# Kernel tuning notes

Measured on AMD Instinct MI355X. Metric: run time of the kernel, lower is better.

The kernel has to match this reference:

```python
import jax, jax.numpy as jnp
import numpy as np

# dims
B, N, D, H, L = 2, 4096, 768, 12, 2
DH = D // H          # 64, equals BigBird block_size
BS = 64              # block size
NB = N // BS         # 64 blocks
R = 3                # num_random_blocks
FF = 4 * D
EPS = 1e-12          # BigBird layer_norm_eps


def _ln(x, g, b):
    mu = jnp.mean(x, -1, keepdims=True)
    var = jnp.mean(jnp.square(x - mu), -1, keepdims=True)
    return (x - mu) * jax.lax.rsqrt(var + EPS) * g + b


def _gelu_new(x):
    c = np.sqrt(2.0 / np.pi).astype(np.float32)
    return 0.5 * x * (1.0 + jnp.tanh(c * (x + 0.044715 * x * x * x)))


def _block_sparse_attn(q, k, v, rb):
    # q,k,v: [B,H,N,DH]; rb: [H,NB,R] random block ids (constant)
    scale = 1.0 / np.sqrt(DH).astype(np.float32)
    qb = q.reshape(B, H, NB, BS, DH)
    kb = k.reshape(B, H, NB, BS, DH)
    vb = v.reshape(B, H, NB, BS, DH)
    M = NB - 2
    mids = jnp.arange(1, NB - 1)
    win = jnp.stack([mids - 1, mids, mids + 1], -1)                    # [M,3]
    glb = jnp.broadcast_to(jnp.array([0, NB - 1], jnp.int32), (M, 2))  # [M,2]
    idx = jnp.concatenate([
        jnp.broadcast_to(glb[None], (H, M, 2)),
        jnp.broadcast_to(win[None], (H, M, 3)),
        rb[:, 1:NB - 1, :]], axis=-1)                                  # [H,M,8]
    hh = jnp.arange(H)[:, None, None]
    # gather key/value blocks: [B,H,M,8,BS,DH] -> [B,H,M,512,DH]
    kg = kb[:, hh, idx].reshape(B, H, M, -1, DH)
    vg = vb[:, hh, idx].reshape(B, H, M, -1, DH)
    qm = qb[:, :, 1:NB - 1]                                            # [B,H,M,BS,DH]
    s = jnp.einsum('bhmqd,bhmkd->bhmqk', qm, kg) * scale
    cm = jnp.einsum('bhmqk,bhmkd->bhmqd', jax.nn.softmax(s, -1), vg)
    # first and last query blocks attend globally (full attention)
    qe = jnp.stack([qb[:, :, 0], qb[:, :, -1]], 2)                     # [B,H,2,BS,DH]
    se = jnp.einsum('bheqd,bhkd->bheqk', qe, k) * scale
    ce = jnp.einsum('bheqk,bhkd->bheqd', jax.nn.softmax(se, -1), v)
    out = jnp.concatenate([ce[:, :, :1], cm, ce[:, :, 1:]], axis=2)    # [B,H,NB,BS,DH]
    return out.reshape(B, H, N, DH)


def _forward(inputs_embeds, rand_blocks, pos_emb, tt_emb, emb_ln_g, emb_ln_b,
             Wq, bq, Wk, bk, Wv, bv, Wo, bo, ln1_g, ln1_b,
             Wi, bi, Wd, bd, ln2_g, ln2_b, fc_w, fc_b):
    x = inputs_embeds + pos_emb[None] + tt_emb                         # embeddings (token_type id 0)
    x = _ln(x, emb_ln_g, emb_ln_b)
    for l in range(L):
        q = (x @ Wq[l] + bq[l]).reshape(B, N, H, DH).transpose(0, 2, 1, 3)
        k = (x @ Wk[l] + bk[l]).reshape(B, N, H, DH).transpose(0, 2, 1, 3)
        v = (x @ Wv[l] + bv[l]).reshape(B, N, H, DH).transpose(0, 2, 1, 3)
        ctx = _block_sparse_attn(q, k, v, rand_blocks[l])
        ctx = ctx.transpose(0, 2, 1, 3).reshape(B, N, D)
        a = _ln(x + ctx @ Wo[l] + bo[l], ln1_g[l], ln1_b[l])
        h = _gelu_new(a @ Wi[l] + bi[l])
        x = _ln(a + h @ Wd[l] + bd[l], ln2_g[l], ln2_b[l])
    pooled = jnp.mean(x, axis=1)                                       # [B,D]; dropout is identity at eval
    return (pooled @ fc_w + fc_b).squeeze()                            # [B]


def setup_inputs() -> dict:
    key = jax.random.key(0)
    ks = jax.random.split(key, 24)
    s = 0.02
    nrm = lambda k, shp: jax.random.normal(k, shp, jnp.float32) * s
    return {
        'inputs_embeds': jax.random.normal(ks[0], (B, N, D), jnp.float32),
        'rand_blocks': jax.random.randint(ks[1], (L, H, NB, R), 0, NB, jnp.int32),
        'pos_emb': nrm(ks[2], (N, D)),
        'tt_emb': nrm(ks[3], (D,)),
        'emb_ln_g': jnp.ones((D,), jnp.float32), 'emb_ln_b': jnp.zeros((D,), jnp.float32),
        'Wq': nrm(ks[4], (L, D, D)), 'bq': jnp.zeros((L, D), jnp.float32),
        'Wk': nrm(ks[5], (L, D, D)), 'bk': jnp.zeros((L, D), jnp.float32),
        'Wv': nrm(ks[6], (L, D, D)), 'bv': jnp.zeros((L, D), jnp.float32),
        'Wo': nrm(ks[7], (L, D, D)), 'bo': jnp.zeros((L, D), jnp.float32),
        'ln1_g': jnp.ones((L, D), jnp.float32), 'ln1_b': jnp.zeros((L, D), jnp.float32),
        'Wi': nrm(ks[8], (L, D, FF)), 'bi': jnp.zeros((L, FF), jnp.float32),
        'Wd': nrm(ks[9], (L, FF, D)), 'bd': jnp.zeros((L, D), jnp.float32),
        'ln2_g': jnp.ones((L, D), jnp.float32), 'ln2_b': jnp.zeros((L, D), jnp.float32),
        'fc_w': nrm(ks[10], (D, 1)), 'fc_b': jnp.zeros((1,), jnp.float32),
    }


def reference(inputs_embeds, rand_blocks, pos_emb, tt_emb, emb_ln_g, emb_ln_b,
              Wq, bq, Wk, bk, Wv, bv, Wo, bo, ln1_g, ln1_b,
              Wi, bi, Wd, bd, ln2_g, ln2_b, fc_w, fc_b):
    return _forward(inputs_embeds, rand_blocks, pos_emb, tt_emb, emb_ln_g, emb_ln_b,
                    Wq, bq, Wk, bk, Wv, bv, Wo, bo, ln1_g, ln1_b,
                    Wi, bi, Wd, bd, ln2_g, ln2_b, fc_w, fc_b)
```

## Files before the change

kernel.cpp:

```cpp
#include <hip/hip_runtime.h>
#include <math.h>

#define B_ 2
#define N_ 4096
#define D_ 768
#define H_ 12
#define DH_ 64
#define NB_ 64
#define FF_ 3072
#define LAYERS_ 2
#define ROWS_ (B_ * N_)

typedef __attribute__((ext_vector_type(8))) short s16x8;
typedef __attribute__((ext_vector_type(8))) unsigned short u16x8;
typedef __attribute__((ext_vector_type(4))) float f32x4;

typedef const __attribute__((address_space(1))) unsigned int ga_u32;
typedef __attribute__((address_space(3))) unsigned int lds_u32;

static __device__ __forceinline__ float gelu_fast(float x) {
    float z2 = 1.5957691216057308f * x * (1.0f + 0.044715f * x * x);
    return x * __builtin_amdgcn_rcpf(1.0f + __expf(-z2));
}

static __device__ __forceinline__ unsigned bf16_rne(float f) {
    unsigned u = __float_as_uint(f);
    return (u + 0x7FFFu + ((u >> 16) & 1u)) >> 16;
}
static __device__ __forceinline__ float bfh2f(unsigned short h) {
    return __uint_as_float(((unsigned)h) << 16);
}

__global__ __launch_bounds__(256)
void prep_weights(const float* __restrict__ Wq, const float* __restrict__ Wk,
                  const float* __restrict__ Wv, const float* __restrict__ Wo,
                  const float* __restrict__ Wi, const float* __restrict__ Wd,
                  unsigned short* __restrict__ Wt) {
    const size_t LW = 7077888;
    int bid = blockIdx.x;
    int l = bid / 1728, r = bid % 1728;
    const float* W; unsigned short* T; int K, N, t, nx;
    if (r < 576) {
        int which = r / 144; t = r % 144; nx = 12; K = 768; N = 768;
        W = (which == 0 ? Wq : which == 1 ? Wk : which == 2 ? Wv : Wo) + (size_t)l * D_ * D_;
        T = Wt + l * LW + (size_t)(which < 3 ? which * 768 * 768 : 2304 * 768);
    } else if (r < 1152) {
        t = r - 576; nx = 48; K = 768; N = 3072;
        W = Wi + (size_t)l * D_ * FF_;
        T = Wt + l * LW + (size_t)(2304 * 768 + 768 * 768);
    } else {
        t = r - 1152; nx = 12; K = 3072; N = 768;
        W = Wd + (size_t)l * FF_ * D_;
        T = Wt + l * LW + (size_t)(2304 * 768 + 768 * 768 + 3072 * 768);
    }
    const int bx = t % nx, by = t / nx;
    __shared__ unsigned short tile[64][72];
    const int k0 = by * 64, n0 = bx * 64;
    const int tt = threadIdx.x;
    const int rr = tt >> 2, c0 = (tt & 3) * 16;
    const float* src = W + (size_t)(k0 + rr) * N + n0 + c0;
#pragma unroll
    for (int j = 0; j < 4; ++j) {
        float4 v = *(const float4*)(src + j * 4);
        tile[rr][c0 + j * 4 + 0] = (unsigned short)bf16_rne(v.x);
        tile[rr][c0 + j * 4 + 1] = (unsigned short)bf16_rne(v.y);
        tile[rr][c0 + j * 4 + 2] = (unsigned short)bf16_rne(v.z);
        tile[rr][c0 + j * 4 + 3] = (unsigned short)bf16_rne(v.w);
    }
    __syncthreads();
    const int nr = tt >> 2, kc = (tt & 3) * 16;
    unsigned short* dst = T + (size_t)(n0 + nr) * K + k0 + kc;
    ushort4 o;
#pragma unroll
    for (int j = 0; j < 4; ++j) {
        o.x = tile[kc + j * 4 + 0][nr];
        o.y = tile[kc + j * 4 + 1][nr];
        o.z = tile[kc + j * 4 + 2][nr];
        o.w = tile[kc + j * 4 + 3][nr];
        *(ushort4*)(dst + j * 4) = o;
    }
}

template <int OMODE>
__global__ __launch_bounds__(256)
void gemm_bt(const unsigned short* __restrict__ A, const unsigned short* __restrict__ Bt,
             const float* __restrict__ bias, void* __restrict__ Cv,
             int N, int K, int gelu) {
    __shared__ __align__(16) unsigned short smem[2 * 8192];
    const int tid = threadIdx.x, lane = tid & 63, wid = tid >> 6;
    const int bid = blockIdx.x;
    const int row0 = (bid & 63) * 128, col0 = (bid >> 6) * 128;
    const int rh = (wid >> 1) * 64, ch = (wid & 1) * 64;
    const int fr = lane & 15, fq = lane >> 4;
    const int srow = wid * 32 + (lane >> 2);
    const int skoff = (lane & 3) * 8;
    const unsigned short* gA0 = A + (size_t)(row0 + srow) * K + skoff;
    const unsigned short* gA1 = gA0 + (size_t)16 * K;
    const unsigned short* gB0 = Bt + (size_t)(col0 + srow) * K + skoff;
    const unsigned short* gB1 = gB0 + (size_t)16 * K;

    f32x4 acc[4][4] = {};
    const int nk = K >> 5;
    {
        unsigned short* s = smem;
        __builtin_amdgcn_global_load_lds((ga_u32*)gA0, (lds_u32*)&s[wid * 1024], 16, 0, 0);
        __builtin_amdgcn_global_load_lds((ga_u32*)gA1, (lds_u32*)&s[wid * 1024 + 512], 16, 0, 0);
        __builtin_amdgcn_global_load_lds((ga_u32*)gB0, (lds_u32*)&s[4096 + wid * 1024], 16, 0, 0);
        __builtin_amdgcn_global_load_lds((ga_u32*)gB1, (lds_u32*)&s[4096 + wid * 1024 + 512], 16, 0, 0);
    }
    for (int kt = 0; kt < nk; ++kt) {
        __syncthreads();
        if (kt + 1 < nk) {
            int k0 = (kt + 1) << 5;
            unsigned short* s = smem + ((kt + 1) & 1) * 8192;
            __builtin_amdgcn_global_load_lds((ga_u32*)(gA0 + k0), (lds_u32*)&s[wid * 1024], 16, 0, 0);
            __builtin_amdgcn_global_load_lds((ga_u32*)(gA1 + k0), (lds_u32*)&s[wid * 1024 + 512], 16, 0, 0);
            __builtin_amdgcn_global_load_lds((ga_u32*)(gB0 + k0), (lds_u32*)&s[4096 + wid * 1024], 16, 0, 0);
            __builtin_amdgcn_global_load_lds((ga_u32*)(gB1 + k0), (lds_u32*)&s[4096 + wid * 1024 + 512], 16, 0, 0);
        }
        const unsigned short* sA = smem + (kt & 1) * 8192;
        const unsigned short* sB = sA + 4096;
        s16x8 af[4], bf[4];
#pragma unroll
        for (int i = 0; i < 4; ++i)
            af[i] = *(const s16x8*)&sA[(rh + 16 * i + fr) * 32 + fq * 8];
#pragma unroll
        for (int j = 0; j < 4; ++j)
            bf[j] = *(const s16x8*)&sB[(ch + 16 * j + fr) * 32 + fq * 8];
#pragma unroll
        for (int i = 0; i < 4; ++i)
#pragma unroll
            for (int j = 0; j < 4; ++j)
                acc[i][j] = __builtin_amdgcn_mfma_f32_16x16x32_bf16(af[i], bf[j], acc[i][j], 0, 0, 0);
    }
    if (OMODE == 0) {
#pragma unroll
        for (int j = 0; j < 4; ++j) {
            int col = col0 + ch + 16 * j + fr;
            float bb = bias[col];
#pragma unroll
            for (int i = 0; i < 4; ++i)
#pragma unroll
                for (int r = 0; r < 4; ++r) {
                    int row = row0 + rh + 16 * i + fq * 4 + r;
                    float v = acc[i][j][r] + bb;
                    if (gelu) v = gelu_fast(v);
                    ((float*)Cv)[(size_t)row * N + col] = v;
                }
        }
    } else {
        unsigned short* sC = smem;
#pragma unroll
        for (int hh = 0; hh < 2; ++hh) {
            __syncthreads();
            if ((wid >> 1) == hh) {
#pragma unroll
                for (int j = 0; j < 4; ++j) {
                    float bb = bias[col0 + ch + 16 * j + fr];
#pragma unroll
                    for (int i = 0; i < 4; ++i)
#pragma unroll
                        for (int r = 0; r < 4; ++r) {
                            float v = acc[i][j][r] + bb;
                            if (gelu) v = gelu_fast(v);
                            sC[(16 * i + fq * 4 + r) * 136 + ch + 16 * j + fr] =
                                (unsigned short)bf16_rne(v);
                        }
                }
            }
            __syncthreads();
#pragma unroll
            for (int p = 0; p < 4; ++p) {
                int seg = p * 256 + tid;
                int r = seg >> 4, c8 = (seg & 15) * 8;
                *(u16x8*)&((unsigned short*)Cv)[(size_t)(row0 + hh * 64 + r) * N + col0 + c8] =
                    *(const u16x8*)&sC[r * 136 + c8];
            }
        }
    }
}

__global__ __launch_bounds__(256)
void gemm_qkv(const unsigned short* __restrict__ A, const unsigned short* __restrict__ Bt,
              const float* __restrict__ bq, const float* __restrict__ bk,
              const float* __restrict__ bv,
              unsigned short* __restrict__ Qh, unsigned short* __restrict__ Kh,
              unsigned short* __restrict__ VT) {
    const int K = D_;
    __shared__ __align__(16) unsigned short smem[2 * 8192];
    const int tid = threadIdx.x, lane = tid & 63, wid = tid >> 6;
    const int bid = blockIdx.x;
    const int row0 = (bid & 63) * 128;
    const int bx = bid >> 6;
    const int col0 = bx * 128;
    const int rh = (wid >> 1) * 64, ch = (wid & 1) * 64;
    const int fr = lane & 15, fq = lane >> 4;
    const int srow = wid * 32 + (lane >> 2);
    const int skoff = (lane & 3) * 8;
    const unsigned short* gA0 = A + (size_t)(row0 + srow) * K + skoff;
    const unsigned short* gA1 = gA0 + (size_t)16 * K;
    const unsigned short* gB0 = Bt + (size_t)(col0 + srow) * K + skoff;
    const unsigned short* gB1 = gB0 + (size_t)16 * K;

    f32x4 acc[4][4] = {};
    const int nk = K >> 5;
    {
        unsigned short* s = smem;
        __builtin_amdgcn_global_load_lds((ga_u32*)gA0, (lds_u32*)&s[wid * 1024], 16, 0, 0);
        __builtin_amdgcn_global_load_lds((ga_u32*)gA1, (lds_u32*)&s[wid * 1024 + 512], 16, 0, 0);
        __builtin_amdgcn_global_load_lds((ga_u32*)gB0, (lds_u32*)&s[4096 + wid * 1024], 16, 0, 0);
        __builtin_amdgcn_global_load_lds((ga_u32*)gB1, (lds_u32*)&s[4096 + wid * 1024 + 512], 16, 0, 0);
    }
    for (int kt = 0; kt < nk; ++kt) {
        __syncthreads();
        if (kt + 1 < nk) {
            int k0 = (kt + 1) << 5;
            unsigned short* s = smem + ((kt + 1) & 1) * 8192;
            __builtin_amdgcn_global_load_lds((ga_u32*)(gA0 + k0), (lds_u32*)&s[wid * 1024], 16, 0, 0);
            __builtin_amdgcn_global_load_lds((ga_u32*)(gA1 + k0), (lds_u32*)&s[wid * 1024 + 512], 16, 0, 0);
            __builtin_amdgcn_global_load_lds((ga_u32*)(gB0 + k0), (lds_u32*)&s[4096 + wid * 1024], 16, 0, 0);
            __builtin_amdgcn_global_load_lds((ga_u32*)(gB1 + k0), (lds_u32*)&s[4096 + wid * 1024 + 512], 16, 0, 0);
        }
        const unsigned short* sA = smem + (kt & 1) * 8192;
        const unsigned short* sB = sA + 4096;
        s16x8 af[4], bf[4];
#pragma unroll
        for (int i = 0; i < 4; ++i)
            af[i] = *(const s16x8*)&sA[(rh + 16 * i + fr) * 32 + fq * 8];
#pragma unroll
        for (int j = 0; j < 4; ++j)
            bf[j] = *(const s16x8*)&sB[(ch + 16 * j + fr) * 32 + fq * 8];
#pragma unroll
        for (int i = 0; i < 4; ++i)
#pragma unroll
            for (int j = 0; j < 4; ++j)
                acc[i][j] = __builtin_amdgcn_mfma_f32_16x16x32_bf16(af[i], bf[j], acc[i][j], 0, 0, 0);
    }
    const int seg = bx / 6;
    const int colbase = col0 - seg * D_;
    const float* bias = (seg == 0) ? bq : (seg == 1) ? bk : bv;
    if (seg == 2) {
#pragma unroll
        for (int j = 0; j < 4; ++j) {
            int col_l = colbase + ch + 16 * j + fr;
            float bb = bias[col_l];
#pragma unroll
            for (int i = 0; i < 4; ++i) {
                int rowbase = row0 + rh + 16 * i + fq * 4;
                ushort4 o;
                o.x = (unsigned short)bf16_rne(acc[i][j][0] + bb);
                o.y = (unsigned short)bf16_rne(acc[i][j][1] + bb);
                o.z = (unsigned short)bf16_rne(acc[i][j][2] + bb);
                o.w = (unsigned short)bf16_rne(acc[i][j][3] + bb);
                *(ushort4*)&VT[(size_t)col_l * ROWS_ + rowbase] = o;
            }
        }
    } else {
        unsigned short* dst = (seg == 0) ? Qh : Kh;
        unsigned short* sC = smem;
#pragma unroll
        for (int hh = 0; hh < 2; ++hh) {
            __syncthreads();
            if ((wid >> 1) == hh) {
#pragma unroll
                for (int j = 0; j < 4; ++j) {
                    float bb = bias[colbase + ch + 16 * j + fr];
#pragma unroll
                    for (int i = 0; i < 4; ++i)
#pragma unroll
                        for (int r = 0; r < 4; ++r)
                            sC[(16 * i + fq * 4 + r) * 136 + ch + 16 * j + fr] =
                                (unsigned short)bf16_rne(acc[i][j][r] + bb);
                }
            }
            __syncthreads();
#pragma unroll
            for (int p = 0; p < 4; ++p) {
                int seg2 = p * 256 + tid;
                int r = seg2 >> 4, c8 = (seg2 & 15) * 8;
                *(u16x8*)&dst[(size_t)(row0 + hh * 64 + r) * D_ + colbase + c8] =
                    *(const u16x8*)&sC[r * 136 + c8];
            }
        }
    }
}

template <bool EDGE>
__global__ __launch_bounds__(256, 4)
void attn_mfma(const unsigned short* __restrict__ Qb, const unsigned short* __restrict__ Kb,
               const unsigned short* __restrict__ VTb, const int* __restrict__ rb,
               unsigned short* __restrict__ ctx, float* __restrict__ scratch) {
    __shared__ __align__(16) unsigned short sQ[64][72];
    __shared__ __align__(16) unsigned short sK[64][72];
    __shared__ __align__(16) unsigned short sVT[64][72];
    __shared__ __align__(16) unsigned short sP[4][16][72];
    __shared__ int sList[16];
    const int tid = threadIdx.x, lane = tid & 63, wid = tid >> 6;
    const int fr = lane & 15, fq = lane >> 4;
    int qb, h, b, nkb, slice = 0;
    if (EDGE) {
        int part = blockIdx.x & 3;
        int hh = (blockIdx.x >> 2) % H_;
        int be = (blockIdx.x >> 2) / H_;
        int eb = be & 1;
        b = be >> 1;
        h = hh;
        qb = eb ? (NB_ - 1) : 0;
        nkb = 16;
        slice = ((b * 2 + eb) * H_ + h) * 4 + part;
        if (tid < 16) sList[tid] = part * 16 + tid;
    } else {
        qb = blockIdx.x % (NB_ - 2) + 1;
        h = (blockIdx.x / (NB_ - 2)) % H_;
        b = blockIdx.x / ((NB_ - 2) * H_);
        nkb = 8;
        if (tid < 8) {
            int e;
            if (tid == 0) e = 0;
            else if (tid == 1) e = NB_ - 1;
            else if (tid < 5) e = qb + (tid - 3);
            else e = rb[(h * NB_ + qb) * 3 + (tid - 5)];
            sList[tid] = e;
        }
    }
    const int qrow0 = b * N_ + qb * 64;
    const unsigned short* Qg = Qb + (size_t)qrow0 * D_ + h * 64;
#pragma unroll
    for (int p = 0; p < 2; ++p) {
        int idx = p * 256 + tid;
        int r = idx >> 3, o = (idx & 7) * 8;
        *(u16x8*)&sQ[r][o] = *(const u16x8*)(Qg + (size_t)r * D_ + o);
    }
    f32x4 oacc[4] = {};
    float l_part[4] = {};
    __syncthreads();
    s16x8 aq0 = *(const s16x8*)&sQ[wid * 16 + fr][fq * 8];
    s16x8 aq1 = *(const s16x8*)&sQ[wid * 16 + fr][32 + fq * 8];

    const int stg_r = tid >> 3, stg_o = (tid & 7) * 8;
    u16x8 kreg[2], vreg[2];
    {
        int keyrow0 = b * N_ + sList[0] * 64;
        const unsigned short* Kg = Kb + (size_t)keyrow0 * D_ + h * 64;
        const unsigned short* Vg = VTb + (size_t)(h * 64) * ROWS_ + keyrow0;
#pragma unroll
        for (int p = 0; p < 2; ++p) {
            int r = stg_r + p * 32;
            kreg[p] = *(const u16x8*)(Kg + (size_t)r * D_ + stg_o);
            vreg[p] = *(const u16x8*)(Vg + (size_t)r * ROWS_ + stg_o);
        }
    }

    for (int kb = 0; kb < nkb; ++kb) {
        __syncthreads();
#pragma unroll
        for (int p = 0; p < 2; ++p) {
            int r = stg_r + p * 32;
            *(u16x8*)&sK[r][stg_o] = kreg[p];
            *(u16x8*)&sVT[r][stg_o] = vreg[p];
        }
        __syncthreads();
        if (kb + 1 < nkb) {
            int keyrow0 = b * N_ + sList[kb + 1] * 64;
            const unsigned short* Kg = Kb + (size_t)keyrow0 * D_ + h * 64;
            const unsigned short* Vg = VTb + (size_t)(h * 64) * ROWS_ + keyrow0;
#pragma unroll
            for (int p = 0; p < 2; ++p) {
                int r = stg_r + p * 32;
                kreg[p] = *(const u16x8*)(Kg + (size_t)r * D_ + stg_o);
                vreg[p] = *(const u16x8*)(Vg + (size_t)r * ROWS_ + stg_o);
            }
        }
#pragma unroll
        for (int g = 0; g < 4; ++g) {
            s16x8 bk0 = *(const s16x8*)&sK[g * 16 + fr][fq * 8];
            s16x8 bk1 = *(const s16x8*)&sK[g * 16 + fr][32 + fq * 8];
            f32x4 s = {};
            s = __builtin_amdgcn_mfma_f32_16x16x32_bf16(aq0, bk0, s, 0, 0, 0);
            s = __builtin_amdgcn_mfma_f32_16x16x32_bf16(aq1, bk1, s, 0, 0, 0);
#pragma unroll
            for (int r = 0; r < 4; ++r) {
                float pv = __expf(s[r] * 0.125f);
                l_part[r] += pv;
                sP[wid][fq * 4 + r][g * 16 + fr] = (unsigned short)bf16_rne(pv);
            }
        }
        s16x8 ap0 = *(const s16x8*)&sP[wid][fr][fq * 8];
        s16x8 ap1 = *(const s16x8*)&sP[wid][fr][32 + fq * 8];
#pragma unroll
        for (int g = 0; g < 4; ++g) {
            s16x8 bv0 = *(const s16x8*)&sVT[g * 16 + fr][fq * 8];
            s16x8 bv1 = *(const s16x8*)&sVT[g * 16 + fr][32 + fq * 8];
            oacc[g] = __builtin_amdgcn_mfma_f32_16x16x32_bf16(ap0, bv0, oacc[g], 0, 0, 0);
            oacc[g] = __builtin_amdgcn_mfma_f32_16x16x32_bf16(ap1, bv1, oacc[g], 0, 0, 0);
        }
    }
    float l4[4];
#pragma unroll
    for (int r = 0; r < 4; ++r) {
        float lv = l_part[r];
        lv += __shfl_xor(lv, 1, 64);
        lv += __shfl_xor(lv, 2, 64);
        lv += __shfl_xor(lv, 4, 64);
        lv += __shfl_xor(lv, 8, 64);
        l4[r] = lv;
    }
    if (EDGE) {
        float* sc = scratch + (size_t)slice * (64 * 64 + 64);
#pragma unroll
        for (int g = 0; g < 4; ++g)
#pragma unroll
            for (int r = 0; r < 4; ++r)
                sc[(wid * 16 + fq * 4 + r) * 64 + g * 16 + fr] = oacc[g][r];
        if (fr == 0) {
#pragma unroll
            for (int r = 0; r < 4; ++r)
                sc[4096 + wid * 16 + fq * 4 + r] = l4[r];
        }
    } else {
        __syncthreads();
#pragma unroll
        for (int g = 0; g < 4; ++g) {
#pragma unroll
            for (int r = 0; r < 4; ++r) {
                float v = oacc[g][r] / l4[r];
                sK[wid * 16 + fq * 4 + r][g * 16 + fr] = (unsigned short)bf16_rne(v);
            }
        }
        __syncthreads();
        unsigned short* Cg = ctx + (size_t)qrow0 * D_ + h * 64;
#pragma unroll
        for (int p = 0; p < 2; ++p) {
            int idx = p * 256 + tid;
            int r = idx >> 3, o = (idx & 7) * 8;
            *(u16x8*)(Cg + (size_t)r * D_ + o) = *(const u16x8*)&sK[r][o];
        }
    }
}

__global__ __launch_bounds__(256)
void edge_combine(const float* __restrict__ scratch, unsigned short* __restrict__ ctx) {
    const int bid = blockIdx.x;
    const int h = bid % H_;
    const int eb = (bid / H_) & 1;
    const int b = bid / (2 * H_);
    const int qb = eb ? (NB_ - 1) : 0;
    const int qrow0 = b * N_ + qb * 64;
    const int slice0 = bid * 4;
    for (int e = threadIdx.x; e < 4096; e += 256) {
        int row = e >> 6, col = e & 63;
        float o = 0.f, l = 0.f;
#pragma unroll
        for (int p = 0; p < 4; ++p) {
            const float* sc = scratch + (size_t)(slice0 + p) * (64 * 64 + 64);
            o += sc[row * 64 + col];
            l += sc[4096 + row];
        }
        ctx[(size_t)(qrow0 + row) * D_ + h * 64 + col] = (unsigned short)bf16_rne(o / l);
    }
}

__global__ __launch_bounds__(256)
void embed_ln_kernel(const float* __restrict__ emb, const float* __restrict__ pos,
                     const float* __restrict__ tt, const float* __restrict__ g,
                     const float* __restrict__ bb, unsigned short* __restrict__ out) {
    __shared__ float red1[4], red2[4];
    const int row = blockIdx.x;
    const int n = row & (N_ - 1);
    const int t = threadIdx.x;
    float v[3];
#pragma unroll
    for (int i = 0; i < 3; ++i) {
        int d = t + i * 256;
        v[i] = emb[(size_t)row * D_ + d] + pos[(size_t)n * D_ + d] + tt[d];
    }
    float s = v[0] + v[1] + v[2];
#pragma unroll
    for (int off = 32; off > 0; off >>= 1) s += __shfl_xor(s, off, 64);
    if ((t & 63) == 0) red1[t >> 6] = s;
    __syncthreads();
    float mu = (red1[0] + red1[1] + red1[2] + red1[3]) * (1.0f / D_);
    float q = 0;
#pragma unroll
    for (int i = 0; i < 3; ++i) { float dv = v[i] - mu; q += dv * dv; }
#pragma unroll
    for (int off = 32; off > 0; off >>= 1) q += __shfl_xor(q, off, 64);
    if ((t & 63) == 0) red2[t >> 6] = q;
    __syncthreads();
    float var = (red2[0] + red2[1] + red2[2] + red2[3]) * (1.0f / D_);
    float rs = rsqrtf(var + 1e-12f);
#pragma unroll
    for (int i = 0; i < 3; ++i) {
        int d = t + i * 256;
        out[(size_t)row * D_ + d] = (unsigned short)bf16_rne((v[i] - mu) * rs * g[d] + bb[d]);
    }
}

__global__ __launch_bounds__(256)
void add_ln_kernel(const unsigned short* __restrict__ X, const unsigned short* __restrict__ Y,
                   const float* __restrict__ g, const float* __restrict__ bb,
                   unsigned short* __restrict__ out) {
    __shared__ float red1[4], red2[4];
    const int row = blockIdx.x;
    const int t = threadIdx.x;
    float v[3];
#pragma unroll
    for (int i = 0; i < 3; ++i) {
        int d = t + i * 256;
        v[i] = bfh2f(X[(size_t)row * D_ + d]) + bfh2f(Y[(size_t)row * D_ + d]);
    }
    float s = v[0] + v[1] + v[2];
#pragma unroll
    for (int off = 32; off > 0; off >>= 1) s += __shfl_xor(s, off, 64);
    if ((t & 63) == 0) red1[t >> 6] = s;
    __syncthreads();
    float mu = (red1[0] + red1[1] + red1[2] + red1[3]) * (1.0f / D_);
    float q = 0;
#pragma unroll
    for (int i = 0; i < 3; ++i) { float dv = v[i] - mu; q += dv * dv; }
#pragma unroll
    for (int off = 32; off > 0; off >>= 1) q += __shfl_xor(q, off, 64);
    if ((t & 63) == 0) red2[t >> 6] = q;
    __syncthreads();
    float var = (red2[0] + red2[1] + red2[2] + red2[3]) * (1.0f / D_);
    float rs = rsqrtf(var + 1e-12f);
#pragma unroll
    for (int i = 0; i < 3; ++i) {
        int d = t + i * 256;
        out[(size_t)row * D_ + d] = (unsigned short)bf16_rne((v[i] - mu) * rs * g[d] + bb[d]);
    }
}

__global__ __launch_bounds__(256)
void pool_partial_kernel(const unsigned short* __restrict__ X, float* __restrict__ partial) {
    int blk = blockIdx.x;
    int b = blk >> 4, c = blk & 15;
    int t = threadIdx.x;
#pragma unroll
    for (int i = 0; i < 3; ++i) {
        int d = t + i * 256;
        float s = 0.f;
        for (int n = 0; n < 256; ++n)
            s += bfh2f(X[((size_t)(b * N_ + c * 256 + n)) * D_ + d]);
        partial[(size_t)(b * 16 + c) * D_ + d] = s;
    }
}

__global__ __launch_bounds__(256)
void pool_final_kernel(const float* __restrict__ partial, const float* __restrict__ fcw,
                       const float* __restrict__ fcb, float* __restrict__ out) {
    __shared__ float red[4];
    int t = threadIdx.x;
    for (int b = 0; b < B_; ++b) {
        float s = 0.f;
#pragma unroll
        for (int i = 0; i < 3; ++i) {
            int d = t + i * 256;
            float ps = 0.f;
#pragma unroll
            for (int c = 0; c < 16; ++c) ps += partial[(size_t)(b * 16 + c) * D_ + d];
            s += ps * (1.0f / N_) * fcw[d];
        }
#pragma unroll
        for (int off = 32; off > 0; off >>= 1) s += __shfl_xor(s, off, 64);
        __syncthreads();
        if ((t & 63) == 0) red[t >> 6] = s;
        __syncthreads();
        if (t == 0) out[b] = red[0] + red[1] + red[2] + red[3] + fcb[0];
    }
}

extern "C" void kernel_launch(void* const* d_in, const int* in_sizes, int n_in,
                              void* d_out, int out_size, void* d_ws, size_t ws_size,
                              hipStream_t stream) {
    (void)in_sizes; (void)n_in; (void)out_size; (void)ws_size;
    const float* emb  = (const float*)d_in[0];
    const int*   rblk = (const int*)d_in[1];
    const float* pos  = (const float*)d_in[2];
    const float* tt   = (const float*)d_in[3];
    const float* elg  = (const float*)d_in[4];
    const float* elb  = (const float*)d_in[5];
    const float* Wq   = (const float*)d_in[6];
    const float* bq   = (const float*)d_in[7];
    const float* Wk   = (const float*)d_in[8];
    const float* bk   = (const float*)d_in[9];
    const float* Wv   = (const float*)d_in[10];
    const float* bv   = (const float*)d_in[11];
    const float* Wo   = (const float*)d_in[12];
    const float* bo   = (const float*)d_in[13];
    const float* ln1g = (const float*)d_in[14];
    const float* ln1b = (const float*)d_in[15];
    const float* Wi   = (const float*)d_in[16];
    const float* bi   = (const float*)d_in[17];
    const float* Wd   = (const float*)d_in[18];
    const float* bd   = (const float*)d_in[19];
    const float* ln2g = (const float*)d_in[20];
    const float* ln2b = (const float*)d_in[21];
    const float* fcw  = (const float*)d_in[22];
    const float* fcb  = (const float*)d_in[23];
    float* outp = (float*)d_out;

    const size_t R = (size_t)ROWS_ * D_;
    float* base = (float*)d_ws;
    unsigned short* Xh  = (unsigned short*)base;
    unsigned short* Abh = (unsigned short*)(base + R / 2);
    unsigned short* Ob  = (unsigned short*)(base + R);
    unsigned short* Qh  = (unsigned short*)(base + 2 * R);
    unsigned short* Kh  = (unsigned short*)(base + 2 * R + R / 2);
    unsigned short* VTh = (unsigned short*)(base + 3 * R);
    unsigned short* Ch  = (unsigned short*)(base + 3 * R + R / 2);
    unsigned short* Hh  = (unsigned short*)(base + 2 * R);
    unsigned short* Wt  = (unsigned short*)(base + 4 * R);
    float* Esc = base + 4 * R + 7077888;
    float* Pp  = Esc + 798720;

    const size_t LW = 7077888;
    const int rows = ROWS_;
    dim3 blk(256);

    prep_weights<<<2 * 1728, blk, 0, stream>>>(Wq, Wk, Wv, Wo, Wi, Wd, Wt);

    embed_ln_kernel<<<rows, blk, 0, stream>>>(emb, pos, tt, elg, elb, Xh);

    for (int l = 0; l < LAYERS_; ++l) {
        const float* bq_l = bq + (size_t)l * D_;
        const float* bk_l = bk + (size_t)l * D_;
        const float* bv_l = bv + (size_t)l * D_;
        const float* bo_l = bo + (size_t)l * D_;
        const float* bi_l = bi + (size_t)l * FF_;
        const float* bd_l = bd + (size_t)l * D_;
        const float* l1g = ln1g + (size_t)l * D_;
        const float* l1b = ln1b + (size_t)l * D_;
        const float* l2g = ln2g + (size_t)l * D_;
        const float* l2b = ln2b + (size_t)l * D_;
        const int* rb_l = rblk + (size_t)l * H_ * NB_ * 3;
        unsigned short* QKVt = Wt + l * LW;
        unsigned short* Ot = QKVt + 2304 * 768;
        unsigned short* It = Ot + 768 * 768;
        unsigned short* Dt = It + 3072 * 768;

        gemm_qkv<<<18 * 64, blk, 0, stream>>>(Xh, QKVt, bq_l, bk_l, bv_l, Qh, Kh, VTh);

        attn_mfma<false><<<B_ * H_ * (NB_ - 2), blk, 0, stream>>>(Qh, Kh, VTh, rb_l, Ch, Esc);
        attn_mfma<true><<<B_ * 2 * H_ * 4, blk, 0, stream>>>(Qh, Kh, VTh, rb_l, Ch, Esc);
        edge_combine<<<B_ * 2 * H_, blk, 0, stream>>>(Esc, Ch);

        gemm_bt<1><<<6 * 64, blk, 0, stream>>>(Ch, Ot, bo_l, Ob, D_, D_, 0);
        add_ln_kernel<<<rows, blk, 0, stream>>>(Xh, Ob, l1g, l1b, Abh);

        gemm_bt<1><<<24 * 64, blk, 0, stream>>>(Abh, It, bi_l, Hh, FF_, D_, 1);
        gemm_bt<1><<<6 * 64, blk, 0, stream>>>(Hh, Dt, bd_l, Ob, D_, FF_, 0);

        add_ln_kernel<<<rows, blk, 0, stream>>>(Abh, Ob, l2g, l2b, Xh);
    }

    pool_partial_kernel<<<B_ * 16, blk, 0, stream>>>(Xh, Pp);
    pool_final_kernel<<<1, blk, 0, stream>>>(Pp, fcw, fcb, outp);
}
```

Before: 752.8 us.

## Add 256x256-tile 512-thread GEMM for FFN up-projection with XCD-aware block swizzle

Adds a new bf16 MFMA GEMM kernel with 256x256 output tiles, 8 waves, double-buffered direct global-to-LDS loads with XOR swizzle, and a block-index remap that groups tiles per XCD. It replaces the 128x128 gemm_bt for the FFN up-projection with GELU. Larger tiles raise arithmetic intensity and cut global traffic per FLOP. The cost is 128KB LDS and heavy register use (128 accumulator floats per lane), which may limit occupancy, and the grid of 384 blocks gives fewer waves to hide latency.

```diff
diff --git a/kernel.cpp b/kernel.cpp
--- a/kernel.cpp
+++ b/kernel.cpp
@@ -176,6 +176,138 @@
                 *(u16x8*)&((unsigned short*)Cv)[(size_t)(row0 + hh * 64 + r) * N + col0 + c8] =
                     *(const u16x8*)&sC[r * 136 + c8];
             }
+        }
+    }
+}
+
+__global__ __launch_bounds__(512, 2)
+void gemm256(const unsigned short* __restrict__ A, const unsigned short* __restrict__ Bt,
+             const float* __restrict__ bias, unsigned short* __restrict__ C,
+             int N, int K, int gelu) {
+    __shared__ __align__(16) unsigned short smem[65536];
+    const int tid = threadIdx.x, lane = tid & 63, wid = tid >> 6;
+    const int fr = lane & 15, fq = lane >> 4;
+    const int rx = fr & 7;
+
+    const int nwg = gridDim.x;
+    const int cpx = nwg >> 3;
+    const int swz = (blockIdx.x & 7) * cpx + (blockIdx.x >> 3);
+    const int ntc = N >> 8;
+    const int rb = swz / ntc, cb = swz % ntc;
+    const int row0 = rb * 256, col0 = cb * 256;
+
+    const int wrow = (wid >> 2) * 128;
+    const int wcol = (wid & 3) * 64;
+
+    const int srow = tid >> 3;
+    const int schunk = tid & 7;
+
+    f32x4 acc[8][4] = {};
+    const int nk = K >> 6;
+
+#define STAGE256(kt_, bs_)                                                          \
+    do {                                                                            \
+        const int koff_ = (kt_) << 6;                                               \
+        _Pragma("unroll")                                                           \
+        for (int p_ = 0; p_ < 4; ++p_) {                                            \
+            int rA_ = p_ * 64 + srow;                                               \
+            int cA_ = (schunk ^ (rA_ & 7)) << 3;                                    \
+            __builtin_amdgcn_global_load_lds(                                       \
+                (ga_u32*)(A + (size_t)(row0 + rA_) * K + koff_ + cA_),              \
+                (lds_u32*)&smem[(bs_) * 32768 + p_ * 4096 + wid * 512], 16, 0, 0);  \
+        }                                                                           \
+        _Pragma("unroll")                                                           \
+        for (int p_ = 0; p_ < 4; ++p_) {                                            \
+            int rB_ = p_ * 64 + srow;                                               \
+            int cB_ = (schunk ^ (rB_ & 7)) << 3;                                    \
+            __builtin_amdgcn_global_load_lds(                                       \
+                (ga_u32*)(Bt + (size_t)(col0 + rB_) * K + koff_ + cB_),             \
+                (lds_u32*)&smem[(bs_) * 32768 + 16384 + p_ * 4096 + wid * 512],     \
+                16, 0, 0);                                                          \
+        }                                                                           \
+    } while (0)
+
+    STAGE256(0, 0);
+    STAGE256(1, 1);
+    asm volatile("s_waitcnt vmcnt(8)" ::: "memory");
+    __builtin_amdgcn_s_barrier();
+    asm volatile("" ::: "memory");
+
+    for (int t = 0; t < nk; ++t) {
+        const int bs = t & 1;
+        const unsigned short* sA = &smem[bs * 32768];
+        const unsigned short* sB = sA + 16384;
+
+        s16x8 a0[8], b0[4];
+#pragma unroll
+        for (int i = 0; i < 8; ++i)
+            a0[i] = *(const s16x8*)&sA[(wrow + 16 * i + fr) * 64 + ((fq ^ rx) << 3)];
+#pragma unroll
+        for (int j = 0; j < 4; ++j)
+            b0[j] = *(const s16x8*)&sB[(wcol + 16 * j + fr) * 64 + ((fq ^ rx) << 3)];
+        __builtin_amdgcn_s_setprio(1);
+#pragma unroll
+        for (int i = 0; i < 8; ++i)
+#pragma unroll
+            for (int j = 0; j < 4; ++j)
+                acc[i][j] = __builtin_amdgcn_mfma_f32_16x16x32_bf16(a0[i], b0[j], acc[i][j], 0, 0, 0);
+        __builtin_amdgcn_s_setprio(0);
+
+        s16x8 a1[8], b1[4];
+#pragma unroll
+        for (int i = 0; i < 8; ++i)
+            a1[i] = *(const s16x8*)&sA[(wrow + 16 * i + fr) * 64 + (((4 + fq) ^ rx) << 3)];
+#pragma unroll
+        for (int j = 0; j < 4; ++j)
+            b1[j] = *(const s16x8*)&sB[(wcol + 16 * j + fr) * 64 + (((4 + fq) ^ rx) << 3)];
+
+        asm volatile("s_waitcnt lgkmcnt(0)" ::: "memory");
+        __builtin_amdgcn_s_barrier();
+        asm volatile("" ::: "memory");
+
+        if (t + 2 < nk) STAGE256(t + 2, bs);
+
+        __builtin_amdgcn_s_setprio(1);
+#pragma unroll
+        for (int i = 0; i < 8; ++i)
+#pragma unroll
+            for (int j = 0; j < 4; ++j)
+                acc[i][j] = __builtin_amdgcn_mfma_f32_16x16x32_bf16(a1[i], b1[j], acc[i][j], 0, 0, 0);
+        __builtin_amdgcn_s_setprio(0);
+
+        if (t + 2 < nk) asm volatile("s_waitcnt vmcnt(8)" ::: "memory");
+        else            asm volatile("s_waitcnt vmcnt(0)" ::: "memory");
+        __builtin_amdgcn_s_barrier();
+        asm volatile("" ::: "memory");
+    }
+#undef STAGE256
+
+    unsigned short* sC = smem;
+#pragma unroll
+    for (int h = 0; h < 2; ++h) {
+        __syncthreads();
+        if ((wid >> 2) == h) {
+#pragma unroll
+            for (int j = 0; j < 4; ++j) {
+                float bb = bias[col0 + wcol + 16 * j + fr];
+#pragma unroll
+                for (int i = 0; i < 8; ++i)
+#pragma unroll
+                    for (int r = 0; r < 4; ++r) {
+                        float v = acc[i][j][r] + bb;
+                        if (gelu) v = gelu_fast(v);
+                        sC[(i * 16 + fq * 4 + r) * 264 + wcol + 16 * j + fr] =
+                            (unsigned short)bf16_rne(v);
+                    }
+            }
+        }
+        __syncthreads();
+#pragma unroll
+        for (int pp = 0; pp < 8; ++pp) {
+            int idx = pp * 512 + tid;
+            int r = idx >> 5, c8 = (idx & 31) * 8;
+            *(u16x8*)&C[(size_t)(row0 + h * 128 + r) * N + col0 + c8] =
+                *(const u16x8*)&sC[r * 264 + c8];
         }
     }
 }
@@ -648,7 +780,8 @@
         gemm_bt<1><<<6 * 64, blk, 0, stream>>>(Ch, Ot, bo_l, Ob, D_, D_, 0);
         add_ln_kernel<<<rows, blk, 0, stream>>>(Xh, Ob, l1g, l1b, Abh);
 
-        gemm_bt<1><<<24 * 64, blk, 0, stream>>>(Abh, It, bi_l, Hh, FF_, D_, 1);
+        gemm256<<<(ROWS_ / 256) * (FF_ / 256), dim3(512), 0, stream>>>(
+            Abh, It, bi_l, Hh, FF_, D_, 1);
         gemm_bt<1><<<6 * 64, blk, 0, stream>>>(Hh, Dt, bd_l, Ob, D_, FF_, 0);
 
         add_ln_kernel<<<rows, blk, 0, stream>>>(Abh, Ob, l2g, l2b, Xh);
```

After: 772.5 us. 1.03x slower.

## Add 256x256-tile pipelined GEMM for FFN up-projection with GELU

Applied to the files above, without the earlier changes.

Introduces a new 512-thread GEMM kernel with 256x256 output tiles, double-buffered direct global-to-LDS loads, XOR-swizzled LDS layout, interleaved staging/MFMA phases with priority hints, and an XCD-aware block swizzle. It replaces the 128x128 gemm_bt for the FF up-projection (8192x3072x768). The larger tile raises arithmetic intensity and data reuse, at the cost of fewer workgroups (384) and large LDS use (128KB), which limits occupancy and may leave CUs underfilled.

```diff
diff --git a/kernel.cpp b/kernel.cpp
--- a/kernel.cpp
+++ b/kernel.cpp
@@ -178,6 +178,169 @@
             }
         }
     }
+}
+
+__global__ __launch_bounds__(512, 2)
+void gemm256(const unsigned short* __restrict__ A, const unsigned short* __restrict__ Bt,
+             const float* __restrict__ bias, unsigned short* __restrict__ C,
+             int N, int K, int gelu) {
+    __shared__ __align__(16) unsigned short smem[65536];
+    const int tid = threadIdx.x, lane = tid & 63, wid = tid >> 6;
+    const int fr = lane & 15, fq = lane >> 4;
+    const int rx = fr & 7;
+
+    const int nwg = gridDim.x;
+    const int cpx = nwg >> 3;
+    const int swz = (blockIdx.x & 7) * cpx + (blockIdx.x >> 3);
+    const int cb = swz >> 5, rb = swz & 31;
+    const int row0 = rb * 256, col0 = cb * 256;
+
+    const int wrow = (wid >> 2) * 128;
+    const int wcol = (wid & 3) * 64;
+
+    const int srow = tid >> 3, schunk = tid & 7;
+    const int scol = (schunk ^ (srow & 7)) << 3;
+    const unsigned short* Ag = A + (size_t)(row0 + srow) * K + scol;
+    const unsigned short* Bg = Bt + (size_t)(col0 + srow) * K + scol;
+
+    const int aoff = (wid >> 2) * 8192 + fr * 64;
+    const int boff = 16384 + ((wid >> 1) & 1) * 8192 + ((wid & 1) * 64 + fr) * 64;
+    const int rc0 = (fq ^ rx) << 3;
+    const int rc1 = ((4 + fq) ^ rx) << 3;
+
+    f32x4 acc[8][4] = {};
+    s16x8 af[4][2], bf[4][2];
+    const int nk = K >> 6, niter = nk >> 1;
+
+#define STG_A(t_, h_)                                                               \
+    do {                                                                            \
+        _Pragma("unroll") for (int c_ = 0; c_ < 2; ++c_)                            \
+            __builtin_amdgcn_global_load_lds(                                       \
+                (ga_u32*)(Ag + (size_t)((h_)*128 + c_*64) * K + ((t_) << 6)),       \
+                (lds_u32*)&smem[((t_)&1)*32768 + (h_)*8192 + c_*4096 + wid*512],    \
+                16, 0, 0);                                                          \
+    } while (0)
+#define STG_B(t_, h_)                                                               \
+    do {                                                                            \
+        _Pragma("unroll") for (int c_ = 0; c_ < 2; ++c_)                            \
+            __builtin_amdgcn_global_load_lds(                                       \
+                (ga_u32*)(Bg + (size_t)((h_)*128 + c_*64) * K + ((t_) << 6)),       \
+                (lds_u32*)&smem[((t_)&1)*32768 + 16384 + (h_)*8192 + c_*4096 + wid*512], \
+                16, 0, 0);                                                          \
+    } while (0)
+#define RD_A(bb_, mh_)                                                              \
+    do {                                                                            \
+        _Pragma("unroll") for (int ii_ = 0; ii_ < 4; ++ii_) {                       \
+            const unsigned short* p_ =                                              \
+                &smem[(bb_)*32768 + aoff + ((mh_)*64 + 16*ii_) * 64];               \
+            af[ii_][0] = *(const s16x8*)(p_ + rc0);                                 \
+            af[ii_][1] = *(const s16x8*)(p_ + rc1);                                 \
+        }                                                                           \
+    } while (0)
+#define RD_B(bb_, j0_)                                                              \
+    do {                                                                            \
+        _Pragma("unroll") for (int jj_ = 0; jj_ < 2; ++jj_) {                       \
+            const unsigned short* p_ =                                              \
+                &smem[(bb_)*32768 + boff + (16*((j0_) + jj_)) * 64];                \
+            bf[(j0_) + jj_][0] = *(const s16x8*)(p_ + rc0);                         \
+            bf[(j0_) + jj_][1] = *(const s16x8*)(p_ + rc1);                         \
+        }                                                                           \
+    } while (0)
+#define MMQ(mh_, nh_)                                                               \
+    do {                                                                            \
+        __builtin_amdgcn_s_setprio(1);                                              \
+        _Pragma("unroll") for (int ii_ = 0; ii_ < 4; ++ii_)                         \
+        _Pragma("unroll") for (int jj_ = 0; jj_ < 2; ++jj_) {                       \
+            acc[4*(mh_)+ii_][2*(nh_)+jj_] = __builtin_amdgcn_mfma_f32_16x16x32_bf16( \
+                af[ii_][0], bf[2*(nh_)+jj_][0], acc[4*(mh_)+ii_][2*(nh_)+jj_], 0, 0, 0); \
+            acc[4*(mh_)+ii_][2*(nh_)+jj_] = __builtin_amdgcn_mfma_f32_16x16x32_bf16( \
+                af[ii_][1], bf[2*(nh_)+jj_][1], acc[4*(mh_)+ii_][2*(nh_)+jj_], 0, 0, 0); \
+        }                                                                           \
+        __builtin_amdgcn_s_setprio(0);                                              \
+    } while (0)
+#define MIDB()                                                                      \
+    do {                                                                            \
+        __builtin_amdgcn_s_barrier();                                               \
+        asm volatile("s_waitcnt lgkmcnt(0)" ::: "memory");                          \
+        __builtin_amdgcn_sched_barrier(0);                                          \
+    } while (0)
+#define ENDB()                                                                      \
+    do {                                                                            \
+        __builtin_amdgcn_s_barrier();                                               \
+        asm volatile("" ::: "memory");                                              \
+    } while (0)
+#define VM4() asm volatile("s_waitcnt vmcnt(4)" ::: "memory")
+#define VM0() asm volatile("s_waitcnt vmcnt(0)" ::: "memory")
+
+    STG_A(0, 0); STG_A(0, 1); STG_B(0, 0); STG_B(0, 1);
+    STG_B(1, 0); STG_B(1, 1);
+    VM4();
+    ENDB();
+
+    for (int i = 0; i < niter - 1; ++i) {
+        const int t0 = 2 * i;
+        RD_A(0, 0); RD_B(0, 0); STG_A(t0 + 1, 0); MIDB(); MMQ(0, 0); ENDB();
+        RD_B(0, 2);             STG_A(t0 + 1, 1); MIDB(); MMQ(0, 1); ENDB();
+        RD_A(0, 1);             STG_B(t0 + 2, 0); MIDB(); MMQ(1, 0); ENDB();
+                                STG_B(t0 + 2, 1); MIDB(); MMQ(1, 1);
+        VM4(); ENDB();
+        RD_A(1, 0); RD_B(1, 0); STG_A(t0 + 2, 0); MIDB(); MMQ(0, 0); ENDB();
+        RD_B(1, 2);             STG_A(t0 + 2, 1); MIDB(); MMQ(0, 1); ENDB();
+        RD_A(1, 1);             STG_B(t0 + 3, 0); MIDB(); MMQ(1, 0); ENDB();
+                                STG_B(t0 + 3, 1); MIDB(); MMQ(1, 1);
+        VM4(); ENDB();
+    }
+    {
+        const int tl = nk - 1;
+        RD_A(0, 0); RD_B(0, 0); STG_A(tl, 0); MIDB(); MMQ(0, 0); ENDB();
+        RD_B(0, 2);             STG_A(tl, 1); MIDB(); MMQ(0, 1); ENDB();
+        RD_A(0, 1);                           MIDB(); MMQ(1, 0); ENDB();
+                                              MIDB(); MMQ(1, 1);
+        VM0(); ENDB();
+        RD_A(1, 0); RD_B(1, 0);               MIDB(); MMQ(0, 0); ENDB();
+        RD_B(1, 2);                           MIDB(); MMQ(0, 1); ENDB();
+        RD_A(1, 1);                           MIDB(); MMQ(1, 0); ENDB();
+                                              MIDB(); MMQ(1, 1); ENDB();
+    }
+#undef STG_A
+#undef STG_B
+#undef RD_A
+#undef RD_B
+#undef MMQ
+#undef MIDB
+#undef ENDB
+#undef VM4
+#undef VM0
+
+    unsigned short* sC = smem;
+#pragma unroll
+    for (int h = 0; h < 2; ++h) {
+        __syncthreads();
+        if ((wid >> 2) == h) {
+#pragma unroll
+            for (int j = 0; j < 4; ++j) {
+                float bb = bias[col0 + wcol + 16 * j + fr];
+#pragma unroll
+                for (int i = 0; i < 8; ++i)
+#pragma unroll
+                    for (int r = 0; r < 4; ++r) {
+                        float v = acc[i][j][r] + bb;
+                        if (gelu) v = gelu_fast(v);
+                        sC[(i * 16 + fq * 4 + r) * 264 + wcol + 16 * j + fr] =
+                            (unsigned short)bf16_rne(v);
+                    }
+            }
+        }
+        __syncthreads();
+#pragma unroll
+        for (int pp = 0; pp < 8; ++pp) {
+            int idx = pp * 512 + tid;
+            int r = idx >> 5, c8 = (idx & 31) * 8;
+            *(u16x8*)&C[(size_t)(row0 + h * 128 + r) * N + col0 + c8] =
+                *(const u16x8*)&sC[r * 264 + c8];
+        }
+    }
+    (void)wrow;
 }
 
 __global__ __launch_bounds__(256)
@@ -648,7 +811,8 @@
         gemm_bt<1><<<6 * 64, blk, 0, stream>>>(Ch, Ot, bo_l, Ob, D_, D_, 0);
         add_ln_kernel<<<rows, blk, 0, stream>>>(Xh, Ob, l1g, l1b, Abh);
 
-        gemm_bt<1><<<24 * 64, blk, 0, stream>>>(Abh, It, bi_l, Hh, FF_, D_, 1);
+        gemm256<<<(ROWS_ / 256) * (FF_ / 256), dim3(512), 0, stream>>>(
+            Abh, It, bi_l, Hh, FF_, D_, 1);
         gemm_bt<1><<<6 * 64, blk, 0, stream>>>(Hh, Dt, bd_l, Ob, D_, FF_, 0);
 
         add_ln_kernel<<<rows, blk, 0, stream>>>(Abh, Ob, l2g, l2b, Xh);
```

New measurement: 793.6 us. +5.4%, slower.
